# Kernel optimization log

Measured on AMD Instinct MI355X. Metric: run time of the kernel, lower is better.

## Reference

```python
import jax, jax.numpy as jnp
import numpy as np

D_MODEL = 1024
NUM_HEADS = 16
D_LATENT = 256
HEAD_DIM = D_MODEL // NUM_HEADS
B, S = 4, 2048


def setup_inputs() -> dict:
    key = jax.random.key(0)
    ks = jax.random.split(key, 11)
    sc_m = 1.0 / np.sqrt(D_MODEL)
    sc_l = 1.0 / np.sqrt(D_LATENT)
    return {
        "x": jax.random.normal(ks[0], (B, S, D_MODEL), dtype=jnp.float32),
        # weights stored as (in, out); equivalent to torch Linear with W^T
        "Wc": jax.random.normal(ks[1], (D_MODEL, D_LATENT), dtype=jnp.float32) * sc_m,
        "bc": jax.random.normal(ks[2], (D_LATENT,), dtype=jnp.float32) * sc_m,
        "Wk": jax.random.normal(ks[3], (D_LATENT, D_MODEL), dtype=jnp.float32) * sc_l,
        "bk": jax.random.normal(ks[4], (D_MODEL,), dtype=jnp.float32) * sc_l,
        "Wv": jax.random.normal(ks[5], (D_LATENT, D_MODEL), dtype=jnp.float32) * sc_l,
        "bv": jax.random.normal(ks[6], (D_MODEL,), dtype=jnp.float32) * sc_l,
        "Wq": jax.random.normal(ks[7], (D_MODEL, D_MODEL), dtype=jnp.float32) * sc_m,
        "bq": jax.random.normal(ks[8], (D_MODEL,), dtype=jnp.float32) * sc_m,
        "Wo": jax.random.normal(ks[9], (D_MODEL, D_MODEL), dtype=jnp.float32) * sc_m,
        "bo": jax.random.normal(ks[10], (D_MODEL,), dtype=jnp.float32) * sc_m,
    }


def reference(x, Wc, bc, Wk, bk, Wv, bv, Wq, bq, Wo, bo):
    b, s, _ = x.shape
    Q = x @ Wq + bq                       # [b,s,d_model]
    kv_latent = x @ Wc + bc               # [b,s,d_latent]
    K = kv_latent @ Wk + bk               # [b,s,d_model]
    V = kv_latent @ Wv + bv               # [b,s,d_model]
    # split heads -> [b,h,s,hd]
    Q = Q.reshape(b, s, NUM_HEADS, HEAD_DIM).transpose(0, 2, 1, 3)
    K = K.reshape(b, s, NUM_HEADS, HEAD_DIM).transpose(0, 2, 1, 3)
    V = V.reshape(b, s, NUM_HEADS, HEAD_DIM).transpose(0, 2, 1, 3)
    scores = jnp.einsum("bhqd,bhkd->bhqk", Q, K) / np.sqrt(HEAD_DIM)
    attn = jax.nn.softmax(scores, axis=-1)  # dropout p=0.0 (eval) -> identity
    out = jnp.einsum("bhqk,bhkd->bhqd", attn, V)
    out = out.transpose(0, 2, 1, 3).reshape(b, s, D_MODEL)
    return out @ Wo + bo
```

## Files before the change

### kernel.cpp

```cpp
#include <hip/hip_runtime.h>

typedef __bf16 bf16;
typedef __bf16 bf16x4 __attribute__((ext_vector_type(4)));
typedef __bf16 bf16x8 __attribute__((ext_vector_type(8)));
typedef float f32x4 __attribute__((ext_vector_type(4)));

#define NHEADS 16
#define HDIM 64
#define SEQ 2048
#define BATCH 4
#define DMODEL 1024
#define NTOK (BATCH * SEQ)
#define KVBLK 64
#define QSCALE 0.18033688f
#define C0EXP  -28.853901f

typedef void gvoid __attribute__((address_space(1)));
typedef void lvoid __attribute__((address_space(3)));

__device__ __forceinline__ f32x4 mfma16(bf16x8 a, bf16x8 b, f32x4 c) {
  return __builtin_amdgcn_mfma_f32_16x16x32_bf16(a, b, c, 0, 0, 0);
}

__device__ __forceinline__ void gload16(const bf16* g, bf16* l) {
  __builtin_amdgcn_global_load_lds((gvoid*)g, (lvoid*)l, 16, 0, 0);
}

__global__ __launch_bounds__(256) void cvt_f32_bf16(
    const float* __restrict__ in, bf16* __restrict__ out, long n) {
  const long i = ((long)blockIdx.x * 256 + threadIdx.x) * 8;
  if (i >= n) return;
  const float4 a = *(const float4*)(in + i);
  const float4 b = *(const float4*)(in + i + 4);
  bf16x8 o;
  o[0] = (bf16)a.x; o[1] = (bf16)a.y; o[2] = (bf16)a.z; o[3] = (bf16)a.w;
  o[4] = (bf16)b.x; o[5] = (bf16)b.y; o[6] = (bf16)b.z; o[7] = (bf16)b.w;
  *(bf16x8*)(out + i) = o;
}

__global__ __launch_bounds__(256) void transpose_cvt(
    const float* __restrict__ in, bf16* __restrict__ out, int K, int N) {
  __shared__ float t[32][33];
  const int n0 = blockIdx.x * 32, k0 = blockIdx.y * 32;
  for (int i = threadIdx.y; i < 32; i += 8)
    t[i][threadIdx.x] = in[(long)(k0 + i) * N + n0 + threadIdx.x];
  __syncthreads();
  for (int i = threadIdx.y; i < 32; i += 8)
    out[(long)(n0 + i) * K + k0 + threadIdx.x] = (bf16)t[threadIdx.x][i];
}

template <int MODE, typename OutT>
__global__ __launch_bounds__(256) void gemm_bt(
    const bf16* __restrict__ A, const bf16* __restrict__ Bt,
    const float* __restrict__ bias, const float* __restrict__ bias2,
    OutT* __restrict__ D, bf16* __restrict__ D2, int N, int K) {
  __shared__ bf16 smem[3 * 4096 * 2];
  bf16* const AsB = smem;
  bf16* const BsB = smem + 3 * 4096;
  const int tid = threadIdx.x;
  const int lane = tid & 63;
  const int wave = tid >> 6;
  const int wr = (wave >> 1) * 64;
  const int wc = (wave & 1) * 64;
  const int r16 = lane & 15;
  const int kg = lane >> 4;
  const long rowBase = (long)blockIdx.x * 128;
  const long colBase = (long)blockIdx.y * 128;

  const int o0 = tid * 16;
  const int o1 = o0 + 4096;
  const int ra0 = o0 >> 6, ra1 = o1 >> 6;
  const int ca0 = ((o0 & 63) ^ (((ra0 >> 1) & 3) << 4)) >> 1;
  const int ca1 = ((o1 & 63) ^ (((ra1 >> 1) & 3) << 4)) >> 1;
  const bf16* pA0 = A + (rowBase + ra0) * K + ca0;
  const bf16* pA1 = A + (rowBase + ra1) * K + ca1;
  const bf16* pB0 = Bt + (colBase + ra0) * K + ca0;
  const bf16* pB1 = Bt + (colBase + ra1) * K + ca1;
  const int e0 = o0 >> 1, e1 = o1 >> 1;

  auto gaddr = [](const bf16* base, int row, int bytecol) -> const bf16* {
    return base + row * 32 + ((bytecol ^ (((row >> 1) & 3) << 4)) >> 1);
  };

  f32x4 acc[4][4] = {};
  const int nk = K >> 5;

#define GSTAGE(kt_)                                        \
  {                                                        \
    const int b_ = (kt_) % 3;                              \
    const int o_ = (kt_) * 32;                             \
    gload16(pA0 + o_, AsB + b_ * 4096 + e0);               \
    gload16(pA1 + o_, AsB + b_ * 4096 + e1);               \
    gload16(pB0 + o_, BsB + b_ * 4096 + e0);               \
    gload16(pB1 + o_, BsB + b_ * 4096 + e1);               \
  }

  GSTAGE(0);
  GSTAGE(1);
  asm volatile("s_waitcnt vmcnt(4)" ::: "memory");
  asm volatile("s_barrier" ::: "memory");

  for (int kt = 0; kt < nk; ++kt) {
    if (kt + 2 < nk) {
      GSTAGE(kt + 2);
      asm volatile("s_waitcnt vmcnt(4)" ::: "memory");
    } else {
      asm volatile("s_waitcnt vmcnt(0)" ::: "memory");
    }
    const bf16* as = AsB + (kt % 3) * 4096;
    const bf16* bs = BsB + (kt % 3) * 4096;
    bf16x8 af[4], bfr[4];
#pragma unroll
    for (int m = 0; m < 4; ++m)
      af[m] = *(const bf16x8*)gaddr(as, wr + m * 16 + r16, kg * 16);
#pragma unroll
    for (int n = 0; n < 4; ++n)
      bfr[n] = *(const bf16x8*)gaddr(bs, wc + n * 16 + r16, kg * 16);
    __builtin_amdgcn_s_setprio(1);
#pragma unroll
    for (int m = 0; m < 4; ++m)
#pragma unroll
      for (int n = 0; n < 4; ++n)
        acc[m][n] = mfma16(af[m], bfr[n], acc[m][n]);
    __builtin_amdgcn_s_setprio(0);
    asm volatile("s_barrier" ::: "memory");
  }
#undef GSTAGE

  if (MODE == 0) {
#pragma unroll
    for (int n = 0; n < 4; ++n) {
      const long col = colBase + wc + n * 16 + r16;
      const float bvv = bias[col];
#pragma unroll
      for (int m = 0; m < 4; ++m) {
        const long row0 = rowBase + wr + m * 16 + kg * 4;
#pragma unroll
        for (int r = 0; r < 4; ++r)
          D[(row0 + r) * N + col] = (OutT)(acc[m][n][r] + bvv);
      }
    }
  } else {
    const bool tr = (MODE == 4) && (colBase >= 1024);
    bf16* E = smem;
#pragma unroll
    for (int n = 0; n < 4; ++n) {
      const int cl = wc + n * 16 + r16;
      const long col = colBase + cl;
      const bool primary = col < 1024;
      const float bvv = primary ? bias[col] : bias2[col - 1024];
#pragma unroll
      for (int m = 0; m < 4; ++m) {
#pragma unroll
        for (int r = 0; r < 4; ++r) {
          const int rl = wr + m * 16 + kg * 4 + r;
          float v = acc[m][n][r] + bvv;
          if (MODE == 3 && primary) v *= QSCALE;
          if (tr) E[cl * 136 + rl] = (bf16)v;
          else    E[rl * 136 + cl] = (bf16)v;
        }
      }
    }
    __syncthreads();
    const int er = tid >> 1;
    const int c0 = (tid & 1) * 64;
    const long brow = rowBase >> 11;
    const int srow = (int)(rowBase & 2047);
    bf16* dp;
    if (!tr) {
      if (colBase < 1024) {
        const long col = colBase + c0;
        dp = D2, dp = nullptr;
        dp = (bf16*)(void*)D +
             (((brow * NHEADS + (col >> 6)) * SEQ) + srow + er) * HDIM;
      } else {
        dp = D2 + (long)(rowBase + er) * 256 + (colBase - 1024) + c0;
      }
    } else {
      const long c2 = colBase - 1024 + er;
      dp = D2 + ((brow * NHEADS + (c2 >> 6)) * HDIM + (c2 & 63)) * SEQ +
           srow + c0;
    }
    const bf16* Er = E + er * 136 + c0;
#pragma unroll
    for (int j = 0; j < 8; ++j)
      *(bf16x8*)(dp + j * 8) = *(const bf16x8*)(Er + j * 8);
  }
}

__global__ __launch_bounds__(512, 4) void mla_attn(
    const bf16* __restrict__ Q, const bf16* __restrict__ Kg,
    const bf16* __restrict__ Vt, bf16* __restrict__ Out) {
  __shared__ bf16 Kl[3][KVBLK * HDIM];
  __shared__ bf16 Vl[3][HDIM * KVBLK];
  __shared__ bf16 Pl[8][32][64];
  const int tid = threadIdx.x;
  const int lane = tid & 63;
  const int w = tid >> 6;
  const int r16 = lane & 15;
  const int kg = lane >> 4;
  const int bid = (int)blockIdx.x;
  const int lb = (bid & 7) * 64 + (bid >> 3);
  const int qb = lb & 7;
  const int bh = lb >> 3;
  const bf16* Qp = Q + (long)bh * SEQ * HDIM;
  const bf16* Kp = Kg + (long)bh * SEQ * HDIM;
  const bf16* Vp = Vt + (long)bh * HDIM * SEQ;
  const int q0 = qb * 256 + w * 32;

  const int so = tid * 16;
  const int srow = so >> 7;
  const int scol = ((so & 127) ^ ((srow & 7) << 4)) >> 1;
  const bf16* KgS = Kp + (long)srow * HDIM + scol;
  const bf16* VgS = Vp + (long)srow * SEQ + scol;
  const int se = so >> 1;

  bf16x8 aq[2][2];
#pragma unroll
  for (int qm = 0; qm < 2; ++qm) {
    const bf16* qp = Qp + (long)(q0 + qm * 16 + r16) * HDIM + kg * 8;
    aq[qm][0] = *(const bf16x8*)qp;
    aq[qm][1] = *(const bf16x8*)(qp + 32);
  }

  f32x4 accO[2][4];
  float psum[2] = {0.f, 0.f};
#pragma unroll
  for (int qm = 0; qm < 2; ++qm)
#pragma unroll
    for (int dt = 0; dt < 4; ++dt) accO[qm][dt] = (f32x4){0.f, 0.f, 0.f, 0.f};
  const f32x4 c0v = {C0EXP, C0EXP, C0EXP, C0EXP};

  auto kaddr = [](const bf16* base, int row, int bytecol) -> const bf16* {
    return base + row * 64 + ((bytecol ^ ((row & 7) << 4)) >> 1);
  };

#define ASTAGE(t_)                                                   \
  {                                                                  \
    const int b_ = (t_) % 3;                                         \
    const long off_ = (long)(t_) * KVBLK;                            \
    gload16(KgS + off_ * HDIM, (bf16*)Kl[b_] + se);                  \
    gload16(VgS + off_, (bf16*)Vl[b_] + se);                         \
  }

  ASTAGE(0);
  ASTAGE(1);
  asm volatile("s_waitcnt vmcnt(2)" ::: "memory");
  asm volatile("s_barrier" ::: "memory");

  const int NT = SEQ / KVBLK;
  for (int t = 0; t < NT; ++t) {
    if (t + 2 < NT) {
      ASTAGE(t + 2);
      asm volatile("s_waitcnt vmcnt(2)" ::: "memory");
    } else {
      asm volatile("s_waitcnt vmcnt(0)" ::: "memory");
    }
    const bf16* kl = Kl[t % 3];
    const bf16* vl = Vl[t % 3];
    f32x4 sc[2][4];
    __builtin_amdgcn_s_setprio(1);
#pragma unroll
    for (int kt = 0; kt < 4; ++kt) {
      const int row = kt * 16 + r16;
      const bf16x8 kf0 = *(const bf16x8*)kaddr(kl, row, kg * 16);
      const bf16x8 kf1 = *(const bf16x8*)kaddr(kl, row, 64 + kg * 16);
#pragma unroll
      for (int qm = 0; qm < 2; ++qm) {
        f32x4 tv = mfma16(kf0, aq[qm][0], c0v);
        tv = mfma16(kf1, aq[qm][1], tv);
        sc[qm][kt] = tv;
      }
    }
    __builtin_amdgcn_s_setprio(0);
#pragma unroll
    for (int qm = 0; qm < 2; ++qm) {
      bf16* prow = &Pl[w][qm * 16 + r16][0];
      const int sw = (r16 & 7) << 4;
#pragma unroll
      for (int kt = 0; kt < 4; ++kt) {
        bf16x4 pk;
#pragma unroll
        for (int r = 0; r < 4; ++r) {
          const float pv = __builtin_amdgcn_exp2f(sc[qm][kt][r]);
          pk[r] = (bf16)pv;
          psum[qm] += pv;
        }
        *(bf16x4*)((char*)prow + ((kt * 32 + kg * 8) ^ sw)) = pk;
      }
    }
    __builtin_amdgcn_s_setprio(1);
#pragma unroll
    for (int kc = 0; kc < 2; ++kc) {
      bf16x8 ap[2];
#pragma unroll
      for (int qm = 0; qm < 2; ++qm) {
        const bf16* prow = &Pl[w][qm * 16 + r16][0];
        const int sw = (r16 & 7) << 4;
        ap[qm] = *(const bf16x8*)((const char*)prow + ((kc * 64 + kg * 16) ^ sw));
      }
#pragma unroll
      for (int dt = 0; dt < 4; ++dt) {
        const int vrow = dt * 16 + r16;
        const bf16x8 vf = *(const bf16x8*)kaddr(vl, vrow, kc * 64 + kg * 16);
        accO[0][dt] = mfma16(ap[0], vf, accO[0][dt]);
        accO[1][dt] = mfma16(ap[1], vf, accO[1][dt]);
      }
    }
    __builtin_amdgcn_s_setprio(0);
    asm volatile("s_barrier" ::: "memory");
  }
#undef ASTAGE

#pragma unroll
  for (int qm = 0; qm < 2; ++qm) {
    psum[qm] += __shfl_xor(psum[qm], 16);
    psum[qm] += __shfl_xor(psum[qm], 32);
  }
  const int b = bh >> 4, h = bh & 15;
#pragma unroll
  for (int qm = 0; qm < 2; ++qm)
#pragma unroll
    for (int r = 0; r < 4; ++r) {
      const float inv = 1.f / __shfl(psum[qm], kg * 4 + r);
      const long qrow = q0 + qm * 16 + kg * 4 + r;
      bf16* op = Out + ((long)b * SEQ + qrow) * DMODEL + h * HDIM;
#pragma unroll
      for (int dt = 0; dt < 4; ++dt)
        op[dt * 16 + r16] = (bf16)(accO[qm][dt][r] * inv);
    }
}

extern "C" void kernel_launch(void* const* d_in, const int* in_sizes, int n_in,
                              void* d_out, int out_size, void* d_ws, size_t ws_size,
                              hipStream_t stream) {
  const float* x  = (const float*)d_in[0];
  const float* Wc = (const float*)d_in[1];
  const float* bc = (const float*)d_in[2];
  const float* Wk = (const float*)d_in[3];
  const float* bk = (const float*)d_in[4];
  const float* Wv = (const float*)d_in[5];
  const float* bv = (const float*)d_in[6];
  const float* Wq = (const float*)d_in[7];
  const float* bq = (const float*)d_in[8];
  const float* Wo = (const float*)d_in[9];
  const float* bo = (const float*)d_in[10];
  float* out = (float*)d_out;

  bf16* p = (bf16*)d_ws;
  bf16* xb   = p; p += (long)NTOK * 1024;
  bf16* WqcT = p; p += 1280 * 1024;
  bf16* WkvT = p; p += 2048 * 256;
  bf16* WoT  = p; p += 1024 * 1024;
  bf16* Qb   = p; p += (long)NTOK * 1024;
  bf16* Kb   = p; p += (long)NTOK * 1024;
  bf16* Vtb  = p; p += (long)NTOK * 1024;
  bf16* Cb   = p; p += (long)NTOK * 256;
  bf16* AO   = xb;

  cvt_f32_bf16<<<(long)NTOK * 1024 / (256 * 8), 256, 0, stream>>>(x, xb, (long)NTOK * 1024);

  dim3 tt(32, 8);
  transpose_cvt<<<dim3(32, 32), tt, 0, stream>>>(Wq, WqcT, 1024, 1024);
  transpose_cvt<<<dim3(8, 32),  tt, 0, stream>>>(Wc, WqcT + 1024 * 1024, 1024, 256);
  transpose_cvt<<<dim3(32, 8),  tt, 0, stream>>>(Wk, WkvT, 256, 1024);
  transpose_cvt<<<dim3(32, 8),  tt, 0, stream>>>(Wv, WkvT + 1024 * 256, 256, 1024);
  transpose_cvt<<<dim3(32, 32), tt, 0, stream>>>(Wo, WoT, 1024, 1024);

  gemm_bt<3, bf16><<<dim3(64, 10), 256, 0, stream>>>(xb, WqcT, bq, bc, Qb, Cb, 1280, 1024);
  gemm_bt<4, bf16><<<dim3(64, 16), 256, 0, stream>>>(Cb, WkvT, bk, bv, Kb, Vtb, 2048, 256);

  mla_attn<<<(SEQ / 256) * BATCH * NHEADS, 512, 0, stream>>>(Qb, Kb, Vtb, AO);

  gemm_bt<0, float><<<dim3(64, 8), 256, 0, stream>>>(AO, WoT, bo, bo, out, (bf16*)nullptr, 1024, 1024);
}
```

Baseline: 185.9 us.

## Give each attention wave 64 query rows with 4 waves per block

The attention block drops from 8 waves with 32 query rows each to 4 waves with 64 query rows each. Every K fragment read from LDS now feeds four query tiles instead of two, and every V fragment feeds four PV MFMAs. Each thread issues two async global-to-LDS loads per K/V stage, and the softmax row sums accumulate as vectors. This aims to cut LDS traffic per MFMA, at the cost of more registers per wave and fewer waves per block to hide latency.

```diff
diff --git a/kernel.cpp b/kernel.cpp
--- a/kernel.cpp
+++ b/kernel.cpp
@@ -170,7 +170,6 @@
     if (!tr) {
       if (colBase < 1024) {
         const long col = colBase + c0;
-        dp = D2, dp = nullptr;
         dp = (bf16*)(void*)D +
              (((brow * NHEADS + (col >> 6)) * SEQ) + srow + er) * HDIM;
       } else {
@@ -188,12 +187,12 @@
   }
 }
 
-__global__ __launch_bounds__(512, 4) void mla_attn(
+__global__ __launch_bounds__(256, 2) void mla_attn(
     const bf16* __restrict__ Q, const bf16* __restrict__ Kg,
     const bf16* __restrict__ Vt, bf16* __restrict__ Out) {
   __shared__ bf16 Kl[3][KVBLK * HDIM];
   __shared__ bf16 Vl[3][HDIM * KVBLK];
-  __shared__ bf16 Pl[8][32][64];
+  __shared__ bf16 Pl[4][64][64];
   const int tid = threadIdx.x;
   const int lane = tid & 63;
   const int w = tid >> 6;
@@ -206,29 +205,35 @@
   const bf16* Qp = Q + (long)bh * SEQ * HDIM;
   const bf16* Kp = Kg + (long)bh * SEQ * HDIM;
   const bf16* Vp = Vt + (long)bh * HDIM * SEQ;
-  const int q0 = qb * 256 + w * 32;
-
-  const int so = tid * 16;
-  const int srow = so >> 7;
-  const int scol = ((so & 127) ^ ((srow & 7) << 4)) >> 1;
-  const bf16* KgS = Kp + (long)srow * HDIM + scol;
-  const bf16* VgS = Vp + (long)srow * SEQ + scol;
-  const int se = so >> 1;
-
-  bf16x8 aq[2][2];
-#pragma unroll
-  for (int qm = 0; qm < 2; ++qm) {
+  const int q0 = qb * 256 + w * 64;
+
+  const int so0 = tid * 16;
+  const int so1 = so0 + 4096;
+  const int sr0 = so0 >> 7, sr1 = so1 >> 7;
+  const int sc0 = ((so0 & 127) ^ ((sr0 & 7) << 4)) >> 1;
+  const int sc1 = ((so1 & 127) ^ ((sr1 & 7) << 4)) >> 1;
+  const bf16* KgS0 = Kp + (long)sr0 * HDIM + sc0;
+  const bf16* KgS1 = Kp + (long)sr1 * HDIM + sc1;
+  const bf16* VgS0 = Vp + (long)sr0 * SEQ + sc0;
+  const bf16* VgS1 = Vp + (long)sr1 * SEQ + sc1;
+  const int se0 = so0 >> 1, se1 = so1 >> 1;
+
+  bf16x8 aq[4][2];
+#pragma unroll
+  for (int qm = 0; qm < 4; ++qm) {
     const bf16* qp = Qp + (long)(q0 + qm * 16 + r16) * HDIM + kg * 8;
     aq[qm][0] = *(const bf16x8*)qp;
     aq[qm][1] = *(const bf16x8*)(qp + 32);
   }
 
-  f32x4 accO[2][4];
-  float psum[2] = {0.f, 0.f};
-#pragma unroll
-  for (int qm = 0; qm < 2; ++qm)
+  f32x4 accO[4][4];
+  f32x4 psumv[4];
+#pragma unroll
+  for (int qm = 0; qm < 4; ++qm) {
+    psumv[qm] = (f32x4){0.f, 0.f, 0.f, 0.f};
 #pragma unroll
     for (int dt = 0; dt < 4; ++dt) accO[qm][dt] = (f32x4){0.f, 0.f, 0.f, 0.f};
+  }
   const f32x4 c0v = {C0EXP, C0EXP, C0EXP, C0EXP};
 
   auto kaddr = [](const bf16* base, int row, int bytecol) -> const bf16* {
@@ -239,62 +244,66 @@
   {                                                                  \
     const int b_ = (t_) % 3;                                         \
     const long off_ = (long)(t_) * KVBLK;                            \
-    gload16(KgS + off_ * HDIM, (bf16*)Kl[b_] + se);                  \
-    gload16(VgS + off_, (bf16*)Vl[b_] + se);                         \
+    gload16(KgS0 + off_ * HDIM, (bf16*)Kl[b_] + se0);                \
+    gload16(KgS1 + off_ * HDIM, (bf16*)Kl[b_] + se1);                \
+    gload16(VgS0 + off_, (bf16*)Vl[b_] + se0);                       \
+    gload16(VgS1 + off_, (bf16*)Vl[b_] + se1);                       \
   }
 
   ASTAGE(0);
   ASTAGE(1);
-  asm volatile("s_waitcnt vmcnt(2)" ::: "memory");
+  asm volatile("s_waitcnt vmcnt(4)" ::: "memory");
   asm volatile("s_barrier" ::: "memory");
 
   const int NT = SEQ / KVBLK;
   for (int t = 0; t < NT; ++t) {
     if (t + 2 < NT) {
       ASTAGE(t + 2);
-      asm volatile("s_waitcnt vmcnt(2)" ::: "memory");
+      asm volatile("s_waitcnt vmcnt(4)" ::: "memory");
     } else {
       asm volatile("s_waitcnt vmcnt(0)" ::: "memory");
     }
     const bf16* kl = Kl[t % 3];
     const bf16* vl = Vl[t % 3];
-    f32x4 sc[2][4];
-    __builtin_amdgcn_s_setprio(1);
+    bf16x8 kf[4][2];
 #pragma unroll
     for (int kt = 0; kt < 4; ++kt) {
       const int row = kt * 16 + r16;
-      const bf16x8 kf0 = *(const bf16x8*)kaddr(kl, row, kg * 16);
-      const bf16x8 kf1 = *(const bf16x8*)kaddr(kl, row, 64 + kg * 16);
-#pragma unroll
-      for (int qm = 0; qm < 2; ++qm) {
-        f32x4 tv = mfma16(kf0, aq[qm][0], c0v);
-        tv = mfma16(kf1, aq[qm][1], tv);
-        sc[qm][kt] = tv;
-      }
-    }
-    __builtin_amdgcn_s_setprio(0);
-#pragma unroll
-    for (int qm = 0; qm < 2; ++qm) {
+      kf[kt][0] = *(const bf16x8*)kaddr(kl, row, kg * 16);
+      kf[kt][1] = *(const bf16x8*)kaddr(kl, row, 64 + kg * 16);
+    }
+#pragma unroll
+    for (int qm = 0; qm < 4; ++qm) {
+      f32x4 sc[4];
+      __builtin_amdgcn_s_setprio(1);
+#pragma unroll
+      for (int kt = 0; kt < 4; ++kt) {
+        f32x4 tv = mfma16(kf[kt][0], aq[qm][0], c0v);
+        tv = mfma16(kf[kt][1], aq[qm][1], tv);
+        sc[kt] = tv;
+      }
+      __builtin_amdgcn_s_setprio(0);
       bf16* prow = &Pl[w][qm * 16 + r16][0];
       const int sw = (r16 & 7) << 4;
 #pragma unroll
       for (int kt = 0; kt < 4; ++kt) {
         bf16x4 pk;
+        f32x4 pv;
 #pragma unroll
         for (int r = 0; r < 4; ++r) {
-          const float pv = __builtin_amdgcn_exp2f(sc[qm][kt][r]);
-          pk[r] = (bf16)pv;
-          psum[qm] += pv;
+          pv[r] = __builtin_amdgcn_exp2f(sc[kt][r]);
+          pk[r] = (bf16)pv[r];
         }
+        psumv[qm] += pv;
         *(bf16x4*)((char*)prow + ((kt * 32 + kg * 8) ^ sw)) = pk;
       }
     }
     __builtin_amdgcn_s_setprio(1);
 #pragma unroll
     for (int kc = 0; kc < 2; ++kc) {
-      bf16x8 ap[2];
-#pragma unroll
-      for (int qm = 0; qm < 2; ++qm) {
+      bf16x8 ap[4];
+#pragma unroll
+      for (int qm = 0; qm < 4; ++qm) {
         const bf16* prow = &Pl[w][qm * 16 + r16][0];
         const int sw = (r16 & 7) << 4;
         ap[qm] = *(const bf16x8*)((const char*)prow + ((kc * 64 + kg * 16) ^ sw));
@@ -303,8 +312,9 @@
       for (int dt = 0; dt < 4; ++dt) {
         const int vrow = dt * 16 + r16;
         const bf16x8 vf = *(const bf16x8*)kaddr(vl, vrow, kc * 64 + kg * 16);
-        accO[0][dt] = mfma16(ap[0], vf, accO[0][dt]);
-        accO[1][dt] = mfma16(ap[1], vf, accO[1][dt]);
+#pragma unroll
+        for (int qm = 0; qm < 4; ++qm)
+          accO[qm][dt] = mfma16(ap[qm], vf, accO[qm][dt]);
       }
     }
     __builtin_amdgcn_s_setprio(0);
@@ -312,17 +322,19 @@
   }
 #undef ASTAGE
 
-#pragma unroll
-  for (int qm = 0; qm < 2; ++qm) {
-    psum[qm] += __shfl_xor(psum[qm], 16);
-    psum[qm] += __shfl_xor(psum[qm], 32);
+  float ps[4];
+#pragma unroll
+  for (int qm = 0; qm < 4; ++qm) {
+    ps[qm] = psumv[qm][0] + psumv[qm][1] + psumv[qm][2] + psumv[qm][3];
+    ps[qm] += __shfl_xor(ps[qm], 16);
+    ps[qm] += __shfl_xor(ps[qm], 32);
   }
   const int b = bh >> 4, h = bh & 15;
 #pragma unroll
-  for (int qm = 0; qm < 2; ++qm)
+  for (int qm = 0; qm < 4; ++qm)
 #pragma unroll
     for (int r = 0; r < 4; ++r) {
-      const float inv = 1.f / __shfl(psum[qm], kg * 4 + r);
+      const float inv = 1.f / __shfl(ps[qm], kg * 4 + r);
       const long qrow = q0 + qm * 16 + kg * 4 + r;
       bf16* op = Out + ((long)b * SEQ + qrow) * DMODEL + h * HDIM;
 #pragma unroll
@@ -370,7 +382,7 @@
   gemm_bt<3, bf16><<<dim3(64, 10), 256, 0, stream>>>(xb, WqcT, bq, bc, Qb, Cb, 1280, 1024);
   gemm_bt<4, bf16><<<dim3(64, 16), 256, 0, stream>>>(Cb, WkvT, bk, bv, Kb, Vtb, 2048, 256);
 
-  mla_attn<<<(SEQ / 256) * BATCH * NHEADS, 512, 0, stream>>>(Qb, Kb, Vtb, AO);
+  mla_attn<<<(SEQ / 256) * BATCH * NHEADS, 256, 0, stream>>>(Qb, Kb, Vtb, AO);
 
   gemm_bt<0, float><<<dim3(64, 8), 256, 0, stream>>>(AO, WoT, bo, bo, out, (bf16*)nullptr, 1024, 1024);
 }
```

Measured after the change: 188.7 us. Within noise of the previous version (+1.5%).
